# Kernel tuning notes

Hardware: AMD Instinct MI355X
Metric: run time of the kernel (lower is better)

Reference implementation:

```python
import jax, jax.numpy as jnp
import numpy as np

NEG_INF = jnp.float32(-2**32 + 1)  # matches the module's padding constant


def setup_inputs() -> dict:
    key = jax.random.key(0)
    ks = jax.random.split(key, 20)
    T, N, E, R = 4, 20000, 320000, 2
    Din, Dh, H = 64, 64, 4
    s = 0.1  # xavier-ish scale
    inp = {
        "x": jax.random.normal(ks[0], (T, N, Din), jnp.float32),
        "edge_index": jax.random.randint(ks[1], (T, R, 2, E), 0, N, jnp.int32),
        "W_src": jax.random.normal(ks[2], (R, Din, H * Dh), jnp.float32) * s,
        "W_dst": jax.random.normal(ks[3], (R, Din, H * Dh), jnp.float32) * s,
        "att_src": jax.random.normal(ks[4], (R, H, Dh), jnp.float32) * s,
        "att_dst": jax.random.normal(ks[5], (R, H, Dh), jnp.float32) * s,
        "ra_W1": jax.random.normal(ks[6], (Dh, 4 * Dh), jnp.float32) * s,
        "ra_b1": jnp.zeros((4 * Dh,), jnp.float32),
        "ra_W2": jax.random.normal(ks[7], (4 * Dh, 1), jnp.float32) * s,
        "lstm_Wih": jax.random.normal(ks[8], (4 * Dh, Dh), jnp.float32) * s,
        "lstm_Whh": jax.random.normal(ks[9], (4 * Dh, Dh), jnp.float32) * s,
        "lstm_bih": jnp.zeros((4 * Dh,), jnp.float32),
        "lstm_bhh": jnp.zeros((4 * Dh,), jnp.float32),
        "pos_emb": jax.random.normal(ks[10], (T, Dh), jnp.float32) * s,
        "Wq": jax.random.normal(ks[11], (Dh, Dh), jnp.float32) * s,
        "Wk": jax.random.normal(ks[12], (Dh, Dh), jnp.float32) * s,
        "Wv": jax.random.normal(ks[13], (Dh, Dh), jnp.float32) * s,
    }
    return inp


def _gat(xt, ei, Ws, Wd, a_s, a_d, N, H, C):
    # PyG GATConv, concat=False, bias=False, eval mode (no dropout)
    src, dst = ei[0], ei[1]
    hs = (xt @ Ws).reshape(N, H, C)
    hd = (xt @ Wd).reshape(N, H, C)
    als = (hs * a_s[None]).sum(-1)          # [N,H]
    ald = (hd * a_d[None]).sum(-1)          # [N,H]
    e = jax.nn.leaky_relu(als[src] + ald[dst], 0.2)   # [E,H]
    m = jax.ops.segment_max(e, dst, num_segments=N)   # [N,H]
    p = jnp.exp(e - m[dst])
    denom = jax.ops.segment_sum(p, dst, num_segments=N)
    alpha = p / (denom[dst] + 1e-16)
    out = jax.ops.segment_sum(hs[src] * alpha[:, :, None], dst, num_segments=N)  # [N,H,C]
    return out.mean(1)                      # concat=False -> mean over heads


def reference(x, edge_index, W_src, W_dst, att_src, att_dst,
              ra_W1, ra_b1, ra_W2,
              lstm_Wih, lstm_Whh, lstm_bih, lstm_bhh,
              pos_emb, Wq, Wk, Wv):
    T, N, _ = x.shape
    R, H, C = att_src.shape   # C == n_hid (per-head GAT channels)

    # ---- intra-relation aggregation: GATConv per etype, vmapped over timeframes
    intra = []
    for r in range(R):
        f = jax.vmap(lambda xt, ei, r=r: _gat(xt, ei, W_src[r], W_dst[r],
                                              att_src[r], att_dst[r], N, H, C))
        intra.append(f(x, edge_index[:, r]))      # [T,N,C]
    h = jnp.stack(intra, axis=2)                  # [T,N,R,C]

    # ---- inter-relation aggregation (RelationAgg), batched over timeframes
    s = jnp.tanh(h @ ra_W1 + ra_b1) @ ra_W2       # [T,N,R,1]
    beta = jax.nn.softmax(s.mean(1), axis=1)      # mean over nodes, softmax over R -> [T,R,1]
    inter = (beta[:, None] * h).sum(2)            # [T,N,C]

    # ---- LSTM over time (batch = nodes)
    def step(carry, xt):
        hh, cc = carry
        g = xt @ lstm_Wih.T + hh @ lstm_Whh.T + lstm_bih + lstm_bhh
        i, f_, gg, o = jnp.split(g, 4, axis=-1)   # torch gate order i,f,g,o
        cc = jax.nn.sigmoid(f_) * cc + jax.nn.sigmoid(i) * jnp.tanh(gg)
        hh = jax.nn.sigmoid(o) * jnp.tanh(cc)
        return (hh, cc), hh
    z = jnp.zeros((N, C), x.dtype)
    _, hs_seq = jax.lax.scan(step, (z, z), inter)  # [T,N,C]
    feats = hs_seq.transpose(1, 0, 2)              # [N,T,C]

    # ---- temporal multi-head attention with causal mask, eval mode
    Ch = C // H
    ti = feats + pos_emb[None]                     # positions are just arange(T)
    qh = (ti @ Wq).reshape(N, T, H, Ch)
    kh = (ti @ Wk).reshape(N, T, H, Ch)
    vh = (ti @ Wv).reshape(N, T, H, Ch)
    scores = jnp.einsum('nqhc,nkhc->nhqk', qh, kh) / jnp.sqrt(jnp.float32(T))
    mask = jnp.tril(jnp.ones((T, T), bool))
    scores = jnp.where(mask[None, None], scores, NEG_INF)
    a = jax.nn.softmax(scores, axis=-1)
    out = jnp.einsum('nhqk,nkhc->nqhc', a, vh).reshape(N, T, C)
    return out  # output_features[ttype][ntype] == out[:, i, :]
```

## Files before the change

### kernel.cpp

```cpp
#include <hip/hip_runtime.h>
#include <hip/hip_bf16.h>

#define T_ 4
#define N_ 20000
#define E_ 320000
#define R_ 2
#define DIN 64
#define G_ 256
#define P_ 8
#define BPAD 16384
#define NB_ 32
#define EPB_ 10000
#define CHN_ 625

typedef unsigned short u16;
typedef __attribute__((ext_vector_type(8))) short bf16x8;
typedef __attribute__((ext_vector_type(2))) _Float16 h2;
typedef __attribute__((ext_vector_type(4))) float f32x4;

__device__ __forceinline__ float bf2f(u16 u) {
    unsigned int i = ((unsigned int)u) << 16; float f;
    __builtin_memcpy(&f, &i, 4); return f;
}
__device__ __forceinline__ u16 f2bf(float f) {
    unsigned int i; __builtin_memcpy(&i, &f, 4);
    unsigned int r = i + 0x7fffu + ((i >> 16) & 1u);
    return (u16)(r >> 16);
}
__device__ __forceinline__ u16 f2h(float f) {
    union { _Float16 h; u16 u; } c; c.h = (_Float16)f; return c.u;
}
__device__ __forceinline__ float sigm(float x) { return 1.f / (1.f + __expf(-x)); }
__device__ __forceinline__ float ftanh(float x) { return 1.f - 2.f / (__expf(2.f * x) + 1.f); }
__device__ __forceinline__ float rdlanef(float v, int l) {
    int i; __builtin_memcpy(&i, &v, 4);
    int r = __builtin_amdgcn_readlane(i, l);
    float f; __builtin_memcpy(&f, &r, 4); return f;
}
__device__ __forceinline__ float fdot2(h2 a, h2 b, float c) {
#if __has_builtin(__builtin_amdgcn_fdot2)
    return __builtin_amdgcn_fdot2(a, b, c, false);
#else
    float r;
    asm("v_dot2_f32_f16 %0, %1, %2, %3" : "=v"(r) : "v"(a), "v"(b), "v"(c));
    return r;
#endif
}
__device__ __forceinline__ unsigned cvtpk_bf16(float lo, float hi) {
    unsigned r;
    asm("v_cvt_pk_bf16_f32 %0, %1, %2" : "=v"(r) : "v"(lo), "v"(hi));
    return r;
}

__device__ __forceinline__ void gemm_direct(
    const u16* __restrict__ A, const u16* __restrict__ Bpad,
    int M, int Astride, int kchunks, int m0, f32x4* acc)
{
    const int tid = threadIdx.x;
    const int lane = tid & 63, wv = tid >> 6;
    const int col = lane & 15, quad = lane >> 4;
    #pragma unroll
    for (int cf = 0; cf < 16; ++cf) { acc[cf][0]=0.f; acc[cf][1]=0.f; acc[cf][2]=0.f; acc[cf][3]=0.f; }

    int row = m0 + wv * 16 + col;
    int row_c = (row < M) ? row : (M - 1);

    for (int kc = 0; kc < kchunks; ++kc) {
        #pragma unroll
        for (int ks = 0; ks < 2; ++ks) {
            bf16x8 a = *(const bf16x8*)(A + (size_t)row_c * Astride + kc * 64 + ks * 32 + quad * 8);
            const u16* bb = Bpad + kc * BPAD + ks * 32 + quad * 8;
            #pragma unroll
            for (int cf = 0; cf < 16; ++cf) {
                bf16x8 b = *(const bf16x8*)(bb + (cf * 16 + col) * 64);
                acc[cf] = __builtin_amdgcn_mfma_f32_16x16x32_bf16(a, b, acc[cf], 0, 0, 0);
            }
        }
    }
}

__global__ __launch_bounds__(256) void k_fold(
    const float* __restrict__ x, const float* __restrict__ wdall,
    float* __restrict__ als_all, float* __restrict__ ald_all, u16* __restrict__ x_h)
{
    __shared__ float wds[1024];
    {
        int tid = threadIdx.x;
        *(float4*)(wds + tid * 4) = *(const float4*)(wdall + tid * 4);
    }
    __syncthreads();

    int t = blockIdx.y;
    int idx = blockIdx.x * 256 + threadIdx.x;
    if (idx >= N_ * 4) return;
    int n = idx >> 2, q = idx & 3;
    const float* xr = x + ((size_t)t * N_ + n) * 64 + q * 16;
    float4 xv[4];
    #pragma unroll
    for (int i = 0; i < 4; ++i) xv[i] = *(const float4*)(xr + i * 4);

    {
        union { u16 h[16]; ushort4 s4[4]; } cv;
        #pragma unroll
        for (int i = 0; i < 4; ++i) {
            cv.h[i*4+0] = f2h(xv[i].x); cv.h[i*4+1] = f2h(xv[i].y);
            cv.h[i*4+2] = f2h(xv[i].z); cv.h[i*4+3] = f2h(xv[i].w);
        }
        u16* xo = x_h + ((size_t)t * N_ + n) * 64 + q * 16;
        #pragma unroll
        for (int i = 0; i < 4; ++i) *(ushort4*)(xo + i * 4) = cv.s4[i];
    }

    float s[16];
    #pragma unroll
    for (int i = 0; i < 16; ++i) s[i] = 0.f;
    #pragma unroll
    for (int i = 0; i < 4; ++i) {
        float xe[4] = {xv[i].x, xv[i].y, xv[i].z, xv[i].w};
        #pragma unroll
        for (int e = 0; e < 4; ++e) {
            int k = q * 16 + i * 4 + e;
            float xk = xe[e];
            #pragma unroll
            for (int tb = 0; tb < 4; ++tb) {
                float4 w = *(const float4*)(wds + tb * 256 + k * 4);
                s[tb*4+0] += xk * w.x; s[tb*4+1] += xk * w.y;
                s[tb*4+2] += xk * w.z; s[tb*4+3] += xk * w.w;
            }
        }
    }
    #pragma unroll
    for (int i = 0; i < 16; ++i) {
        s[i] += __shfl_xor(s[i], 1);
        s[i] += __shfl_xor(s[i], 2);
    }
    if (q == 0) {
        *(float4*)(als_all + ((size_t)(t*2+0) * N_ + n) * 4) = make_float4(s[0], s[1], s[2], s[3]);
        *(float4*)(als_all + ((size_t)(t*2+1) * N_ + n) * 4) = make_float4(s[4], s[5], s[6], s[7]);
        *(float4*)(ald_all + ((size_t)(t*2+0) * N_ + n) * 4) = make_float4(s[8], s[9], s[10], s[11]);
        *(float4*)(ald_all + ((size_t)(t*2+1) * N_ + n) * 4) = make_float4(s[12], s[13], s[14], s[15]);
    }
}

__global__ void k_prep(const float* __restrict__ Wdst, const float* __restrict__ att_dst,
                       const float* __restrict__ Wih, const float* __restrict__ Whh,
                       const float* __restrict__ bih, const float* __restrict__ bhh,
                       const float* __restrict__ Wsrc, const float* __restrict__ att_src,
                       const float* __restrict__ raW1,
                       const float* __restrict__ Wq, const float* __restrict__ Wk,
                       const float* __restrict__ Wv,
                       float* __restrict__ wdall, float* __restrict__ biasv,
                       u16* __restrict__ raW1_pad, u16* __restrict__ Wc_pad,
                       u16* __restrict__ qkv_pad, u16* __restrict__ postB_pad,
                       float* __restrict__ sspart)
{
    int tid = threadIdx.x, bid = blockIdx.x;
    if (bid == 0) {
        for (int i = tid; i < 1024; i += 256) sspart[i] = 0.f;
        int k = tid >> 2, h = tid & 3;
        for (int r = 0; r < 2; ++r) {
            float ss = 0.f, sd = 0.f;
            for (int c = 0; c < 64; ++c) {
                ss += Wsrc[((size_t)r * 64 + k) * 256 + h * 64 + c] * att_src[r * 256 + h * 64 + c];
                sd += Wdst[((size_t)r * 64 + k) * 256 + h * 64 + c] * att_dst[r * 256 + h * 64 + c];
            }
            wdall[r * 256 + k * 4 + h] = ss;
            wdall[512 + r * 256 + k * 4 + h] = sd;
        }
        biasv[tid] = bih[tid] + bhh[tid];
    }
    for (int i = bid * 256 + tid; i < BPAD; i += gridDim.x * 256) {
        int n = i >> 6, kk = i & 63;
        raW1_pad[i] = f2bf(raW1[kk * 256 + n]);
    }
    for (int i = bid * 256 + tid; i < 2 * BPAD; i += gridDim.x * 256) {
        int kc = i >> 14, q = i & (BPAD - 1), n = q >> 6, kk = q & 63;
        const float* W = kc ? Whh : Wih;
        Wc_pad[i] = f2bf(W[n * 64 + kk]);
    }
    for (int i = bid * 256 + tid; i < 192 * 64; i += gridDim.x * 256) {
        int g = i >> 6, kk = i & 63;
        int j = g >> 6, c = g & 63;
        const float* W = (j == 0) ? Wq : (j == 1) ? Wk : Wv;
        qkv_pad[i] = f2bf(W[kk * 64 + c]);
    }
    for (int i = bid * 256 + tid; i < 2 * 4 * 4096; i += gridDim.x * 256) {
        int r = i >> 14, q = i & 16383, kc = q >> 12, qq = q & 4095;
        int c = qq >> 6, kk = qq & 63;
        int d = kc * 16 + (kk >> 2), h = kk & 3;
        postB_pad[i] = f2bf(Wsrc[(size_t)r * 16384 + d * 256 + h * 64 + c]);
    }
}

__global__ __launch_bounds__(256) void k_hist(const int* __restrict__ ei,
                                              u16* __restrict__ rank, u16* __restrict__ partial)
{
    __shared__ unsigned int hist[N_ / 2];
    int b = blockIdx.x, p = blockIdx.y, tid = threadIdx.x;
    for (int i = tid; i < N_ / 2; i += 256) hist[i] = 0u;
    __syncthreads();
    const int* dsts = ei + ((size_t)p * 2 + 1) * E_ + b * EPB_;
    u16* rk = rank + (size_t)p * E_ + b * EPB_;
    for (int e = tid; e < EPB_; e += 256) {
        int dst = dsts[e];
        unsigned sh = (unsigned)(dst & 1) * 16u;
        unsigned old = atomicAdd(&hist[dst >> 1], 1u << sh);
        rk[e] = (u16)((old >> sh) & 0xffffu);
    }
    __syncthreads();
    u16* part = partial + ((size_t)p * NB_ + b) * N_;
    for (int n = tid; n < N_; n += 256) {
        unsigned hv = hist[n >> 1];
        part[n] = (u16)((hv >> ((unsigned)(n & 1) * 16u)) & 0xffffu);
    }
}

__global__ __launch_bounds__(256) void k_scan1(u16* __restrict__ partial,
                                               int* __restrict__ offsets, int* __restrict__ chunktot)
{
    int p = blockIdx.y, ch = blockIdx.x;
    int tid = threadIdx.x, lane = tid & 63, wid = tid >> 6;
    __shared__ int wtot[4];
    u16* part = partial + (size_t)p * NB_ * N_;
    int* ofs = offsets + (size_t)p * (N_ + 1);
    int n0 = ch * CHN_;
    int carry = 0;
    for (int rnd = 0; rnd < 3; ++rnd) {
        int i = rnd * 256 + tid;
        int n = n0 + i;
        int v = 0;
        if (i < CHN_) {
            int run = 0;
            #pragma unroll 8
            for (int b = 0; b < NB_; ++b) {
                int pv = part[b * N_ + n];
                part[b * N_ + n] = (u16)run;
                run += pv;
            }
            v = run;
        }
        int incl = v;
        for (int d = 1; d < 64; d <<= 1) { int u = __shfl_up(incl, d); if (lane >= d) incl += u; }
        if (lane == 63) wtot[wid] = incl;
        __syncthreads();
        if (tid < 4) {
            int iv = wtot[tid];
            for (int d = 1; d < 4; d <<= 1) { int u = __shfl_up(iv, d); if (tid >= d) iv += u; }
            wtot[tid] = iv;
        }
        __syncthreads();
        int woff = (wid > 0) ? wtot[wid - 1] : 0;
        int tot = wtot[3];
        int excl = carry + woff + incl - v;
        if (i < CHN_) ofs[n] = excl;
        carry += tot;
        __syncthreads();
    }
    if (tid == 0) chunktot[p * NB_ + ch] = carry;
}

__global__ void k_scan3(int* __restrict__ offsets, const int* __restrict__ chunktot) {
    __shared__ int cb[NB_];
    int p = blockIdx.y;
    int tid = threadIdx.x;
    if (tid < 64) {
        int v = (tid < NB_) ? chunktot[p * NB_ + tid] : 0;
        #pragma unroll
        for (int d = 1; d < NB_; d <<= 1) { int u = __shfl_up(v, d); if (tid >= d) v += u; }
        if (tid < NB_) cb[tid] = v;
    }
    __syncthreads();
    int n = blockIdx.x * 256 + tid;
    if (n < N_) {
        int c = n / CHN_;
        int base = (c > 0) ? cb[c - 1] : 0;
        offsets[(size_t)p * (N_ + 1) + n] += base;
    }
    if (n == 0)
        offsets[(size_t)p * (N_ + 1) + N_] = E_;
}

__global__ void k_scatter(const int* __restrict__ ei, const int* __restrict__ offsets,
                          const u16* __restrict__ rank, const u16* __restrict__ partial,
                          u16* __restrict__ csr) {
    int bid = blockIdx.x;
    int p = bid & 7;
    int e = (bid >> 3) * 256 + threadIdx.x;
    int src = ei[((size_t)p * 2 + 0) * E_ + e];
    int dst = ei[((size_t)p * 2 + 1) * E_ + e];
    int b = e / EPB_;
    int pos = offsets[p * (N_ + 1) + dst]
            + (int)partial[((size_t)p * NB_ + b) * N_ + dst]
            + (int)rank[(size_t)p * E_ + e];
    csr[(size_t)p * E_ + pos] = (u16)src;
}

__global__ __launch_bounds__(256) void k_agg(
    const int* __restrict__ offsets, const u16* __restrict__ csr,
    const float* __restrict__ als_all, const float* __restrict__ ald_all,
    const u16* __restrict__ x_h, const u16* __restrict__ postB_pad,
    u16* __restrict__ intra)
{
    __shared__ __align__(16) u16 ptab[4][4][64];
    __shared__ __align__(16) u16 xs[16 * 256];
    const int bid = blockIdx.x;
    const int p = bid & 7;
    const int t = p >> 1, rel = p & 1;
    const int* off   = offsets + (size_t)p * (N_ + 1);
    const u16* srcs  = csr + (size_t)p * E_;
    const float* als = als_all + (size_t)p * N_ * 4;
    const float* ald = ald_all + (size_t)p * N_ * 4;
    const u16* xb    = x_h + (size_t)t * N_ * 64;

    const int tid = threadIdx.x, lane = tid & 63, wv = tid >> 6;
    const int g = lane >> 4, el = lane & 15;
    const int nb0 = (bid >> 3) * 16;
    const int n0 = nb0 + wv * 4;
    const int ng = n0 + g;
    const int o0 = off[ng], o1 = off[ng + 1];
    const int deg = o1 - o0;
    const float4 aldv = *(const float4*)(ald + (size_t)ng * 4);
    u16* pt = &ptab[wv][0][0];
    const int pw = g * 64 + (el >> 1) * 8 + (el & 1);

    int sdeg[4];
    #pragma unroll
    for (int q = 0; q < 4; ++q) sdeg[q] = __builtin_amdgcn_readlane(deg, q * 16);
    int mdeg = max(max(sdeg[0], sdeg[1]), max(sdeg[2], sdeg[3]));
    int nrounds = (mdeg + 15) >> 4;

    float acc[4][4];
    #pragma unroll
    for (int q = 0; q < 4; ++q)
        #pragma unroll
        for (int h = 0; h < 4; ++h) acc[q][h] = 0.f;
    float d0 = 0.f, d1 = 0.f, d2 = 0.f, d3 = 0.f;

    for (int rr = 0; rr < nrounds; ++rr) {
        int e = rr * 16 + el;
        int sv = 0;
        float p0 = 0.f, p1 = 0.f, p2 = 0.f, p3 = 0.f;
        if (e < deg) {
            sv = (int)srcs[o0 + e];
            float4 av = *(const float4*)(als + (size_t)sv * 4);
            float e0 = av.x + aldv.x, e1 = av.y + aldv.y;
            float e2 = av.z + aldv.z, e3 = av.w + aldv.w;
            e0 = fmaxf(e0, 0.2f * e0); e1 = fmaxf(e1, 0.2f * e1);
            e2 = fmaxf(e2, 0.2f * e2); e3 = fmaxf(e3, 0.2f * e3);
            p0 = __expf(e0); p1 = __expf(e1); p2 = __expf(e2); p3 = __expf(e3);
        }
        d0 += p0; d1 += p1; d2 += p2; d3 += p3;
        pt[pw + 0] = f2h(p0); pt[pw + 2] = f2h(p1);
        pt[pw + 4] = f2h(p2); pt[pw + 6] = f2h(p3);
        #pragma unroll
        for (int q = 0; q < 4; ++q) {
            int rem = sdeg[q] - rr * 16;
            if (rem >= 16) {
                const u16* ptq = pt + q * 64;
                unsigned xl0[8], xl1[8];
                #pragma unroll
                for (int pr = 0; pr < 8; ++pr) {
                    int s0i = __builtin_amdgcn_readlane(sv, q * 16 + pr * 2);
                    int s1i = __builtin_amdgcn_readlane(sv, q * 16 + pr * 2 + 1);
                    xl0[pr] = xb[((size_t)(unsigned)s0i << 6) + lane];
                    xl1[pr] = xb[((size_t)(unsigned)s1i << 6) + lane];
                }
                #pragma unroll
                for (int pr = 0; pr < 8; ++pr) {
                    unsigned xp = xl0[pr] | (xl1[pr] << 16);
                    uint4 ppv = *(const uint4*)(ptq + pr * 8);
                    h2 xv, q0, q1, q2, q3;
                    __builtin_memcpy(&xv, &xp, 4);
                    __builtin_memcpy(&q0, &ppv.x, 4);
                    __builtin_memcpy(&q1, &ppv.y, 4);
                    __builtin_memcpy(&q2, &ppv.z, 4);
                    __builtin_memcpy(&q3, &ppv.w, 4);
                    acc[q][0] = fdot2(xv, q0, acc[q][0]);
                    acc[q][1] = fdot2(xv, q1, acc[q][1]);
                    acc[q][2] = fdot2(xv, q2, acc[q][2]);
                    acc[q][3] = fdot2(xv, q3, acc[q][3]);
                }
            } else if (rem > 0) {
                const u16* ptq = pt + q * 64;
                unsigned xl0[8], xl1[8];
                #pragma unroll
                for (int pr = 0; pr < 8; ++pr) {
                    if (pr * 2 < rem) {
                        int s0i = __builtin_amdgcn_readlane(sv, q * 16 + pr * 2);
                        int s1i = __builtin_amdgcn_readlane(sv, q * 16 + pr * 2 + 1);
                        xl0[pr] = xb[((size_t)(unsigned)s0i << 6) + lane];
                        xl1[pr] = xb[((size_t)(unsigned)s1i << 6) + lane];
                    }
                }
                #pragma unroll
                for (int pr = 0; pr < 8; ++pr) {
                    if (pr * 2 < rem) {
                        unsigned xp = xl0[pr] | (xl1[pr] << 16);
                        uint4 ppv = *(const uint4*)(ptq + pr * 8);
                        h2 xv, q0, q1, q2, q3;
                        __builtin_memcpy(&xv, &xp, 4);
                        __builtin_memcpy(&q0, &ppv.x, 4);
                        __builtin_memcpy(&q1, &ppv.y, 4);
                        __builtin_memcpy(&q2, &ppv.z, 4);
                        __builtin_memcpy(&q3, &ppv.w, 4);
                        acc[q][0] = fdot2(xv, q0, acc[q][0]);
                        acc[q][1] = fdot2(xv, q1, acc[q][1]);
                        acc[q][2] = fdot2(xv, q2, acc[q][2]);
                        acc[q][3] = fdot2(xv, q3, acc[q][3]);
                    }
                }
            }
        }
    }
    d0 += __shfl_xor(d0, 1); d0 += __shfl_xor(d0, 2);
    d0 += __shfl_xor(d0, 4); d0 += __shfl_xor(d0, 8);
    d1 += __shfl_xor(d1, 1); d1 += __shfl_xor(d1, 2);
    d1 += __shfl_xor(d1, 4); d1 += __shfl_xor(d1, 8);
    d2 += __shfl_xor(d2, 1); d2 += __shfl_xor(d2, 2);
    d2 += __shfl_xor(d2, 4); d2 += __shfl_xor(d2, 8);
    d3 += __shfl_xor(d3, 1); d3 += __shfl_xor(d3, 2);
    d3 += __shfl_xor(d3, 4); d3 += __shfl_xor(d3, 8);
    float inv0 = 0.25f / (d0 + 1e-16f);
    float inv1 = 0.25f / (d1 + 1e-16f);
    float inv2 = 0.25f / (d2 + 1e-16f);
    float inv3 = 0.25f / (d3 + 1e-16f);
    #pragma unroll
    for (int q = 0; q < 4; ++q) {
        float s0 = rdlanef(inv0, q * 16);
        float s1 = rdlanef(inv1, q * 16);
        float s2 = rdlanef(inv2, q * 16);
        float s3 = rdlanef(inv3, q * 16);
        unsigned w01 = cvtpk_bf16(acc[q][0] * s0, acc[q][1] * s1);
        unsigned w23 = cvtpk_bf16(acc[q][2] * s2, acc[q][3] * s3);
        int rowt = wv * 4 + q;
        char* dst = (char*)xs + rowt * 512 + (((lane >> 1) ^ (rowt & 7)) * 16) + (lane & 1) * 8;
        *(uint2*)dst = make_uint2(w01, w23);
    }
    __syncthreads();

    {
        const int col = lane & 15, quad = lane >> 4;
        const u16* Bp = postB_pad + (size_t)rel * 4 * 4096;
        f32x4 pacc;
        pacc[0] = 0.f; pacc[1] = 0.f; pacc[2] = 0.f; pacc[3] = 0.f;
        #pragma unroll
        for (int kc = 0; kc < 4; ++kc) {
            #pragma unroll
            for (int ks = 0; ks < 2; ++ks) {
                int slot = kc * 8 + ks * 4 + quad;
                bf16x8 a = *(const bf16x8*)((const char*)xs + col * 512 + ((slot ^ (col & 7)) * 16));
                bf16x8 b = *(const bf16x8*)(Bp + (size_t)kc * 4096 + (wv * 16 + col) * 64 + ks * 32 + quad * 8);
                pacc = __builtin_amdgcn_mfma_f32_16x16x32_bf16(a, b, pacc, 0, 0, 0);
            }
        }
        #pragma unroll
        for (int reg = 0; reg < 4; ++reg) {
            int node = nb0 + quad * 4 + reg;
            intra[(((size_t)t * N_ + node) * 2 + rel) * 64 + wv * 16 + col] = f2bf(pacc[reg]);
        }
    }
}

__global__ __launch_bounds__(256) void k_relagg(
    const u16* __restrict__ A, const u16* __restrict__ W1pad, const float* __restrict__ b1,
    const float* __restrict__ W2, float* __restrict__ sspart)
{
    int m0 = blockIdx.x * 64;
    f32x4 acc[16];
    gemm_direct(A, W1pad, T_ * N_ * R_, 64, 1, m0, acc);

    const int tid = threadIdx.x, lane = tid & 63, wv = tid >> 6;
    const int col = lane & 15;
    float sp[4] = {0.f, 0.f, 0.f, 0.f};
    #pragma unroll
    for (int cf = 0; cf < 16; ++cf) {
        int gcol = cf * 16 + col;
        float bb = b1[gcol];
        float ww = W2[gcol];
        #pragma unroll
        for (int reg = 0; reg < 4; ++reg)
            sp[reg] += ftanh(acc[cf][reg] + bb) * ww;
    }
    #pragma unroll
    for (int reg = 0; reg < 4; ++reg) {
        float v = sp[reg];
        v += __shfl_xor(v, 1); v += __shfl_xor(v, 2);
        v += __shfl_xor(v, 4); v += __shfl_xor(v, 8);
        sp[reg] = v;
    }
    float se = sp[0] + sp[2];
    float so = sp[1] + sp[3];
    se += __shfl_xor(se, 16); se += __shfl_xor(se, 32);
    so += __shfl_xor(so, 16); so += __shfl_xor(so, 32);
    __shared__ float red[8];
    if (lane == 0) { red[wv * 2] = se; red[wv * 2 + 1] = so; }
    __syncthreads();
    if (tid == 0) {
        float s0 = red[0] + red[2] + red[4] + red[6];
        float s1 = red[1] + red[3] + red[5] + red[7];
        int t = m0 / (N_ * R_);
        float* line = sspart + (blockIdx.x & 63) * 16;
        atomicAdd(&line[t * 2 + 0], s0);
        atomicAdd(&line[t * 2 + 1], s1);
    }
}

__global__ __launch_bounds__(256) void k_lstm(
    const u16* __restrict__ intra, const float* __restrict__ sspart,
    const u16* __restrict__ Wc_pad, const float* __restrict__ biasv,
    u16* __restrict__ feats)
{
    __shared__ __align__(16) u16 wtab[512][64];
    __shared__ __align__(16) u16 hl[64][72];
    __shared__ float betas_s[8];
    const int tid = threadIdx.x, lane = tid & 63, wv = tid >> 6;
    const int col = lane & 15, quad = lane >> 4;
    int m0 = blockIdx.x * 64;
    int row = m0 + wv * 16 + col;
    int row_c = (row < N_) ? row : (N_ - 1);
    int rowbase = m0 + wv * 16 + quad * 4;

    bf16x8 pi[4][4];
    #pragma unroll
    for (int t = 0; t < 4; ++t) {
        const u16* ib = intra + ((size_t)t * N_ + row_c) * 128;
        #pragma unroll
        for (int k = 0; k < 4; ++k)
            pi[t][k] = *(const bf16x8*)(ib + k * 32 + quad * 8);
    }

    {
        const uint4* src = (const uint4*)Wc_pad;
        #pragma unroll
        for (int it = 0; it < 16; ++it) {
            int u = it * 256 + tid;
            int r = u >> 3, s = u & 7;
            uint4 v = src[u];
            *(uint4*)((char*)&wtab[0][0] + (size_t)r * 128 + ((s ^ (r & 7)) * 16)) = v;
        }
    }
    if (tid < 64) {
        float a8[8];
        #pragma unroll
        for (int s = 0; s < 8; ++s) a8[s] = sspart[tid * 16 + s];
        #pragma unroll
        for (int s = 0; s < 8; ++s) {
            float v = a8[s];
            v += __shfl_xor(v, 1); v += __shfl_xor(v, 2);
            v += __shfl_xor(v, 4); v += __shfl_xor(v, 8);
            v += __shfl_xor(v, 16); v += __shfl_xor(v, 32);
            a8[s] = v;
        }
        if (tid < 4) {
            float s0 = a8[tid * 2] * (1.f / N_), s1 = a8[tid * 2 + 1] * (1.f / N_);
            float mx = fmaxf(s0, s1);
            float e0 = __expf(s0 - mx), e1 = __expf(s1 - mx);
            float inv = 1.f / (e0 + e1);
            betas_s[tid * 2] = e0 * inv; betas_s[tid * 2 + 1] = e1 * inv;
        }
    }
    __syncthreads();
    float betas[8];
    #pragma unroll
    for (int i = 0; i < 8; ++i) betas[i] = betas_s[i];

    float cc[4][4];
    #pragma unroll
    for (int j = 0; j < 4; ++j)
        #pragma unroll
        for (int reg = 0; reg < 4; ++reg) cc[j][reg] = 0.f;

    const int c7 = col & 7;
    #pragma unroll
    for (int t = 0; t < 4; ++t) {
        float b0 = betas[t * 2], b1 = betas[t * 2 + 1];

        f32x4 acc[16];
        #pragma unroll
        for (int cf = 0; cf < 16; ++cf) { acc[cf][0]=0.f; acc[cf][1]=0.f; acc[cf][2]=0.f; acc[cf][3]=0.f; }

        #pragma unroll
        for (int ks = 0; ks < 2; ++ks) {
            bf16x8 i0 = pi[t][ks];
            bf16x8 i1 = pi[t][2 + ks];
            union { u16 h[8]; bf16x8 v; } cv;
            #pragma unroll
            for (int j = 0; j < 8; ++j)
                cv.h[j] = f2bf(b0 * bf2f((u16)i0[j]) + b1 * bf2f((u16)i1[j]));
            #pragma unroll
            for (int cf = 0; cf < 16; ++cf) {
                bf16x8 b = *(const bf16x8*)((const char*)&wtab[0][0]
                    + (size_t)(cf * 16 + col) * 128 + (((ks * 4 + quad) ^ c7) * 16));
                acc[cf] = __builtin_amdgcn_mfma_f32_16x16x32_bf16(cv.v, b, acc[cf], 0, 0, 0);
            }
        }
        if (t > 0) {
            #pragma unroll
            for (int ks = 0; ks < 2; ++ks) {
                bf16x8 a = *(const bf16x8*)&hl[wv * 16 + col][ks * 32 + quad * 8];
                #pragma unroll
                for (int cf = 0; cf < 16; ++cf) {
                    bf16x8 b = *(const bf16x8*)((const char*)&wtab[0][0]
                        + (size_t)(256 + cf * 16 + col) * 128 + (((ks * 4 + quad) ^ c7) * 16));
                    acc[cf] = __builtin_amdgcn_mfma_f32_16x16x32_bf16(a, b, acc[cf], 0, 0, 0);
                }
            }
        }

        #pragma unroll
        for (int j = 0; j < 4; ++j) {
            int c = j * 16 + col;
            float bi = biasv[c], bf_ = biasv[64 + c], bg = biasv[128 + c], bo = biasv[192 + c];
            #pragma unroll
            for (int reg = 0; reg < 4; ++reg) {
                float gi = acc[j][reg] + bi;
                float gf = acc[j + 4][reg] + bf_;
                float gg = acc[j + 8][reg] + bg;
                float go = acc[j + 12][reg] + bo;
                float c2 = sigm(gf) * cc[j][reg] + sigm(gi) * ftanh(gg);
                float hh = sigm(go) * ftanh(c2);
                cc[j][reg] = c2;
                u16 hb = f2bf(hh);
                hl[wv * 16 + quad * 4 + reg][c] = hb;
                int rr = rowbase + reg;
                if (rr < N_)
                    feats[(size_t)rr * 256 + t * 64 + c] = hb;
            }
        }
    }
}

__global__ __launch_bounds__(256) void k_attn(
    const u16* __restrict__ feats, const float* __restrict__ pos_emb,
    const u16* __restrict__ qkv_pad, float* __restrict__ out)
{
    __shared__ float qkv_s[64 * 200];
    const int tid = threadIdx.x, lane = tid & 63, wv = tid >> 6;
    const int col = lane & 15, quad = lane >> 4;
    int m0 = blockIdx.x * 64;
    int row = m0 + wv * 16 + col;
    int trow = row & 3;

    f32x4 acc[12];
    #pragma unroll
    for (int cf = 0; cf < 12; ++cf) { acc[cf][0]=0.f; acc[cf][1]=0.f; acc[cf][2]=0.f; acc[cf][3]=0.f; }
    #pragma unroll
    for (int ks = 0; ks < 2; ++ks) {
        int coff = ks * 32 + quad * 8;
        bf16x8 fv = *(const bf16x8*)(feats + (size_t)row * 64 + coff);
        float4 p0 = *(const float4*)(pos_emb + trow * 64 + coff);
        float4 p1 = *(const float4*)(pos_emb + trow * 64 + coff + 4);
        union { u16 h[8]; bf16x8 v; } cv;
        cv.h[0] = f2bf(bf2f((u16)fv[0]) + p0.x); cv.h[1] = f2bf(bf2f((u16)fv[1]) + p0.y);
        cv.h[2] = f2bf(bf2f((u16)fv[2]) + p0.z); cv.h[3] = f2bf(bf2f((u16)fv[3]) + p0.w);
        cv.h[4] = f2bf(bf2f((u16)fv[4]) + p1.x); cv.h[5] = f2bf(bf2f((u16)fv[5]) + p1.y);
        cv.h[6] = f2bf(bf2f((u16)fv[6]) + p1.z); cv.h[7] = f2bf(bf2f((u16)fv[7]) + p1.w);
        bf16x8 a = cv.v;
        const u16* bb = qkv_pad + ks * 32 + quad * 8;
        #pragma unroll
        for (int cf = 0; cf < 12; ++cf) {
            bf16x8 b = *(const bf16x8*)(bb + (cf * 16 + col) * 64);
            acc[cf] = __builtin_amdgcn_mfma_f32_16x16x32_bf16(a, b, acc[cf], 0, 0, 0);
        }
    }
    #pragma unroll
    for (int cf = 0; cf < 12; ++cf) {
        int g = cf * 16 + col;
        #pragma unroll
        for (int reg = 0; reg < 4; ++reg) {
            int rl = wv * 16 + quad * 4 + reg;
            qkv_s[rl * 200 + g] = acc[cf][reg];
        }
    }
    __syncthreads();

    int nl = wv * 4 + (lane >> 4);
    int sub = lane & 15;
    int h = sub >> 2, tq = sub & 3;
    const float* qrow = qkv_s + (nl * 4 + tq) * 200 + h * 16;

    float s[4];
    #pragma unroll
    for (int tk = 0; tk < 4; ++tk) {
        const float* krow = qkv_s + (nl * 4 + tk) * 200 + 64 + h * 16;
        float d = 0.f;
        #pragma unroll
        for (int j = 0; j < 16; ++j) d += qrow[j] * krow[j];
        s[tk] = (tk > tq) ? -4294967295.0f : d * 0.5f;
    }
    float mx = fmaxf(fmaxf(s[0], s[1]), fmaxf(s[2], s[3]));
    float a0 = __expf(s[0]-mx), a1 = __expf(s[1]-mx), a2 = __expf(s[2]-mx), a3 = __expf(s[3]-mx);
    float inv = 1.f / (a0 + a1 + a2 + a3);
    a0 *= inv; a1 *= inv; a2 *= inv; a3 *= inv;

    int n = blockIdx.x * 16 + nl;
    const float* v0 = qkv_s + (nl * 4 + 0) * 200 + 128 + h * 16;
    const float* v1 = v0 + 200, *v2 = v0 + 400, *v3 = v0 + 600;
    #pragma unroll
    for (int cc4 = 0; cc4 < 4; ++cc4) {
        float4 o;
        o.x = a0*v0[cc4*4+0] + a1*v1[cc4*4+0] + a2*v2[cc4*4+0] + a3*v3[cc4*4+0];
        o.y = a0*v0[cc4*4+1] + a1*v1[cc4*4+1] + a2*v2[cc4*4+1] + a3*v3[cc4*4+1];
        o.z = a0*v0[cc4*4+2] + a1*v1[cc4*4+2] + a2*v2[cc4*4+2] + a3*v3[cc4*4+2];
        o.w = a0*v0[cc4*4+3] + a1*v1[cc4*4+3] + a2*v2[cc4*4+3] + a3*v3[cc4*4+3];
        *(float4*)(out + (size_t)n * 256 + tq * 64 + h * 16 + cc4 * 4) = o;
    }
}

extern "C" void kernel_launch(void* const* d_in, const int* in_sizes, int n_in,
                              void* d_out, int out_size, void* d_ws, size_t ws_size,
                              hipStream_t stream) {
    const float* x     = (const float*)d_in[0];
    const int* ei      = (const int*)d_in[1];
    const float* Wsrc  = (const float*)d_in[2];
    const float* Wdst  = (const float*)d_in[3];
    const float* att_src = (const float*)d_in[4];
    const float* att_dst = (const float*)d_in[5];
    const float* raW1  = (const float*)d_in[6];
    const float* rab1  = (const float*)d_in[7];
    const float* raW2  = (const float*)d_in[8];
    const float* Wih   = (const float*)d_in[9];
    const float* Whh   = (const float*)d_in[10];
    const float* bih   = (const float*)d_in[11];
    const float* bhh   = (const float*)d_in[12];
    const float* pos   = (const float*)d_in[13];
    const float* Wq    = (const float*)d_in[14];
    const float* Wk    = (const float*)d_in[15];
    const float* Wv    = (const float*)d_in[16];
    float* out = (float*)d_out;

    char* w = (char*)d_ws;
    size_t off = 0;
    auto alloc = [&](size_t bytes) -> char* {
        char* pp = w + off; off += (bytes + 255) & ~(size_t)255; return pp;
    };
    u16*   intra     = (u16*)  alloc((size_t)T_ * N_ * R_ * 64 * 2);
    u16*   x_h       = (u16*)  alloc((size_t)T_ * N_ * 64 * 2);
    float* sspart    = (float*)alloc(1024 * 4);
    float* wdall     = (float*)alloc(1024 * 4);
    float* biasv     = (float*)alloc(256 * 4);
    u16*   raW1_pad  = (u16*)  alloc(BPAD * 2);
    u16*   Wc_pad    = (u16*)  alloc(2 * BPAD * 2);
    u16*   qkv_pad   = (u16*)  alloc(192 * 64 * 2);
    u16*   postB_pad = (u16*)  alloc(2 * 4 * 4096 * 2);
    int*   chunktot  = (int*)  alloc(P_ * NB_ * 4);
    char*  ubase   = alloc(0);
    size_t uoff = 0;
    auto ualloc = [&](size_t bytes) -> char* {
        char* pp = ubase + uoff; uoff += (bytes + 255) & ~(size_t)255; return pp;
    };
    int*   offsets = (int*)  ualloc((size_t)P_ * (N_ + 1) * 4);
    u16*   csr     = (u16*)  ualloc((size_t)P_ * E_ * 2);
    float* als_all = (float*)ualloc((size_t)P_ * N_ * 4 * 4);
    float* ald_all = (float*)ualloc((size_t)P_ * N_ * 4 * 4);
    u16*   partial = (u16*)  ualloc((size_t)P_ * NB_ * N_ * 2);
    u16*   rank    = (u16*)  ualloc((size_t)P_ * E_ * 2);
    u16*   feats   = (u16*)  ubase;
    (void)ws_size; (void)in_sizes; (void)n_in; (void)out_size;

    k_prep<<<72, 256, 0, stream>>>(Wdst, att_dst, Wih, Whh, bih, bhh, Wsrc, att_src, raW1,
                                   Wq, Wk, Wv, wdall, biasv, raW1_pad, Wc_pad, qkv_pad,
                                   postB_pad, sspart);
    k_hist<<<dim3(NB_, 8), 256, 0, stream>>>(ei, rank, partial);
    k_scan1<<<dim3(NB_, 8), 256, 0, stream>>>(partial, offsets, chunktot);
    k_scan3<<<dim3(79, 8), 256, 0, stream>>>(offsets, chunktot);
    k_scatter<<<10000, 256, 0, stream>>>(ei, offsets, rank, partial, csr);
    k_fold<<<dim3(313, 4), 256, 0, stream>>>(x, wdall, als_all, ald_all, x_h);
    k_agg<<<10000, 256, 0, stream>>>(offsets, csr, als_all, ald_all, x_h, postB_pad, intra);
    k_relagg<<<2500, 256, 0, stream>>>(intra, raW1_pad, rab1, raW2, sspart);
    k_lstm<<<313, 256, 0, stream>>>(intra, sspart, Wc_pad, biasv, feats);
    k_attn<<<1250, 256, 0, stream>>>(feats, pos, qkv_pad, out);
}
```

Baseline: 397.9 us.

## Double-buffer attention weights in k_agg and prefetch next round's edge data

Computes the next round's source indices and exp attention weights into a second LDS buffer while the current round's gather and dot products run, so the als gather latency overlaps the x gathers. It also merges the full-round and partial-round branches into one guarded path, and adds a min-blocks hint of 6 to launch_bounds. The exchange is more registers and LDS per wave and the loss of the unguarded fast path for full rounds. The min-blocks hint may force register spilling.

```diff
diff --git a/kernel.cpp b/kernel.cpp
--- a/kernel.cpp
+++ b/kernel.cpp
@@ -295,13 +295,13 @@
     csr[(size_t)p * E_ + pos] = (u16)src;
 }
 
-__global__ __launch_bounds__(256) void k_agg(
+__global__ __launch_bounds__(256, 6) void k_agg(
     const int* __restrict__ offsets, const u16* __restrict__ csr,
     const float* __restrict__ als_all, const float* __restrict__ ald_all,
     const u16* __restrict__ x_h, const u16* __restrict__ postB_pad,
     u16* __restrict__ intra)
 {
-    __shared__ __align__(16) u16 ptab[4][4][64];
+    __shared__ __align__(16) u16 ptab[4][2][256];
     __shared__ __align__(16) u16 xs[16 * 256];
     const int bid = blockIdx.x;
     const int p = bid & 7;
@@ -320,7 +320,6 @@
     const int o0 = off[ng], o1 = off[ng + 1];
     const int deg = o1 - o0;
     const float4 aldv = *(const float4*)(ald + (size_t)ng * 4);
-    u16* pt = &ptab[wv][0][0];
     const int pw = g * 64 + (el >> 1) * 8 + (el & 1);
 
     int sdeg[4];
@@ -336,7 +335,7 @@
         for (int h = 0; h < 4; ++h) acc[q][h] = 0.f;
     float d0 = 0.f, d1 = 0.f, d2 = 0.f, d3 = 0.f;
 
-    for (int rr = 0; rr < nrounds; ++rr) {
+    auto pphase = [&](int rr, int buf) -> int {
         int e = rr * 16 + el;
         int sv = 0;
         float p0 = 0.f, p1 = 0.f, p2 = 0.f, p3 = 0.f;
@@ -350,44 +349,29 @@
             p0 = __expf(e0); p1 = __expf(e1); p2 = __expf(e2); p3 = __expf(e3);
         }
         d0 += p0; d1 += p1; d2 += p2; d3 += p3;
+        u16* pt = &ptab[wv][buf][0];
         pt[pw + 0] = f2h(p0); pt[pw + 2] = f2h(p1);
         pt[pw + 4] = f2h(p2); pt[pw + 6] = f2h(p3);
+        return sv;
+    };
+
+    int cur = 0;
+    int sv_cur = (nrounds > 0) ? pphase(0, 0) : 0;
+    for (int rr = 0; rr < nrounds; ++rr) {
+        int sv_nxt = 0;
+        if (rr + 1 < nrounds) sv_nxt = pphase(rr + 1, cur ^ 1);
+        const u16* ptb = &ptab[wv][cur][0];
         #pragma unroll
         for (int q = 0; q < 4; ++q) {
             int rem = sdeg[q] - rr * 16;
-            if (rem >= 16) {
-                const u16* ptq = pt + q * 64;
-                unsigned xl0[8], xl1[8];
-                #pragma unroll
-                for (int pr = 0; pr < 8; ++pr) {
-                    int s0i = __builtin_amdgcn_readlane(sv, q * 16 + pr * 2);
-                    int s1i = __builtin_amdgcn_readlane(sv, q * 16 + pr * 2 + 1);
-                    xl0[pr] = xb[((size_t)(unsigned)s0i << 6) + lane];
-                    xl1[pr] = xb[((size_t)(unsigned)s1i << 6) + lane];
-                }
-                #pragma unroll
-                for (int pr = 0; pr < 8; ++pr) {
-                    unsigned xp = xl0[pr] | (xl1[pr] << 16);
-                    uint4 ppv = *(const uint4*)(ptq + pr * 8);
-                    h2 xv, q0, q1, q2, q3;
-                    __builtin_memcpy(&xv, &xp, 4);
-                    __builtin_memcpy(&q0, &ppv.x, 4);
-                    __builtin_memcpy(&q1, &ppv.y, 4);
-                    __builtin_memcpy(&q2, &ppv.z, 4);
-                    __builtin_memcpy(&q3, &ppv.w, 4);
-                    acc[q][0] = fdot2(xv, q0, acc[q][0]);
-                    acc[q][1] = fdot2(xv, q1, acc[q][1]);
-                    acc[q][2] = fdot2(xv, q2, acc[q][2]);
-                    acc[q][3] = fdot2(xv, q3, acc[q][3]);
-                }
-            } else if (rem > 0) {
-                const u16* ptq = pt + q * 64;
+            if (rem > 0) {
+                const u16* ptq = ptb + q * 64;
                 unsigned xl0[8], xl1[8];
                 #pragma unroll
                 for (int pr = 0; pr < 8; ++pr) {
                     if (pr * 2 < rem) {
-                        int s0i = __builtin_amdgcn_readlane(sv, q * 16 + pr * 2);
-                        int s1i = __builtin_amdgcn_readlane(sv, q * 16 + pr * 2 + 1);
+                        int s0i = __builtin_amdgcn_readlane(sv_cur, q * 16 + pr * 2);
+                        int s1i = __builtin_amdgcn_readlane(sv_cur, q * 16 + pr * 2 + 1);
                         xl0[pr] = xb[((size_t)(unsigned)s0i << 6) + lane];
                         xl1[pr] = xb[((size_t)(unsigned)s1i << 6) + lane];
                     }
@@ -411,6 +395,8 @@
                 }
             }
         }
+        sv_cur = sv_nxt;
+        cur ^= 1;
     }
     d0 += __shfl_xor(d0, 1); d0 += __shfl_xor(d0, 2);
     d0 += __shfl_xor(d0, 4); d0 += __shfl_xor(d0, 8);
```

Measured after the change: 389.5 us. 2.1% less time.
